# Kernel tuning notes

Measured on AMD Instinct MI355X. Metric: run time of the kernel, lower is better.

## Reference

```python
import jax, jax.numpy as jnp
import numpy as np

# dims
B, S, E, H, W = 32, 256, 512, 512, 512   # batch, max_sentence_length, word_emb, rnn_units, weight_size
ENC = 2 * H                               # bidirectional encoder hidden
V = 50000                                 # vocab


def setup_inputs() -> dict:
    key = jax.random.key(0)
    ks = jax.random.split(key, 16)
    n = jax.random.normal
    return {
        "word_ids": jax.random.randint(ks[0], (B, S), 0, V),
        "encoder_outputs": n(ks[1], (B, S, ENC), jnp.float32),
        "encoder_hn": n(ks[2], (B, H), jnp.float32),          # initial decoder cell state
        "emb": n(ks[3], (V, E), jnp.float32) * 0.02,          # WordFeature embedding table
        "chunk_emb": n(ks[4], (S, W), jnp.float32) * 0.02,    # chunk_length_embedding
        "W1": n(ks[5], (ENC, W), jnp.float32) / np.sqrt(ENC),
        "W2": n(ks[6], (E, W), jnp.float32) / np.sqrt(E),
        "W3": n(ks[7], (E, W), jnp.float32) / np.sqrt(E),
        "W4": n(ks[8], (H, W), jnp.float32) / np.sqrt(H),
        "vt1": n(ks[9], (W,), jnp.float32) / np.sqrt(W),
        "vt2": n(ks[10], (W,), jnp.float32) / np.sqrt(W),
        "Wx": n(ks[11], (E, 4 * H), jnp.float32) / np.sqrt(E),  # decoder LSTM cell
        "Wh": n(ks[12], (H, 4 * H), jnp.float32) / np.sqrt(H),
        "bias": jnp.zeros((4 * H,), jnp.float32),
    }


def reference(word_ids, encoder_outputs, encoder_hn, emb, chunk_emb,
              W1, W2, W3, W4, vt1, vt2, Wx, Wh, bias):
    Ss = word_ids.shape[1]
    Hh = encoder_hn.shape[1]
    inp = emb[word_ids]                                   # [B,S,E] word features
    b1 = jnp.einsum('bse,ew->bsw', encoder_outputs, W1)   # W1(encoder_output), hoisted
    b2 = jnp.einsum('bse,ew->bsw', inp, W2)               # W2(single_input), hoisted
    pos = jnp.arange(Ss)

    def decode_one(inp_b, b1_b, b2_b, c0):
        def step(carry, _):
            last_bond, bond, h, c, out_vec = carry
            done = bond >= Ss
            # decoder input: mean of current segment inp[last_bond:bond] (zeros at step 0)
            m = ((pos >= last_bond) & (pos < bond)).astype(inp_b.dtype)  # [S]
            x = (m @ inp_b) / jnp.maximum(m.sum(), 1.0)                  # [E]
            # LSTM cell (stand-in for decoder.pointer_forward)
            gates = x @ Wx + h @ Wh + bias                               # [4H]
            i_g, f_g, g_g, o_g = jnp.split(gates, 4)
            c_n = jax.nn.sigmoid(f_g) * c + jax.nn.sigmoid(i_g) * jnp.tanh(g_g)
            h_n = jax.nn.sigmoid(o_g) * jnp.tanh(c_n)
            h2 = jnp.where(done, h, h_n)
            c2 = jnp.where(done, c, c_n)
            bidx = jnp.minimum(bond, Ss - 1)
            # pointer attention over positions >= bond
            blend = jnp.tanh(b1_b + b2_b + inp_b[bidx] @ W3 + h2 @ W4)   # [S,W]
            seg_len = jnp.clip(bond - last_bond, 0, Ss - 1)
            scores = blend @ vt1 + chunk_emb[seg_len] @ vt2              # [S]
            scores = jnp.where(pos >= bidx, scores, -1e30)
            # log_softmax is monotonic -> argmax of scores == argmax of log-probs
            idx = jnp.argmax(scores)                                     # absolute = max_index + bond
            new_bond = jnp.where(idx > bond, idx, bond + 1)              # force progress
            widx = jnp.minimum(new_bond, Ss - 1)
            val = jnp.where((~done) & (new_bond < Ss), 1.0, out_vec[widx])
            out_new = out_vec.at[widx].set(val)
            last2 = jnp.where(done, last_bond, bond)
            bond2 = jnp.where(done, bond, new_bond)
            return (last2, bond2, h2, c2, out_new), None

        init = (jnp.int32(0), jnp.int32(0),
                jnp.zeros((Hh,), inp_b.dtype), c0,
                jnp.zeros((Ss,), inp_b.dtype))
        (_, _, _, _, out_vec), _ = jax.lax.scan(step, init, None, length=Ss)
        return out_vec

    outs = jax.vmap(decode_one)(inp, b1, b2, encoder_hn)   # [B,S]
    return outs.T                                          # [S,B] == torch.stack(output_list, 1)
```

## Files before the change

kernel.cpp:

```cpp
#include <hip/hip_runtime.h>
#include <math.h>

#define Bn   32
#define Sn   256
#define En   512
#define Hn   512
#define Wn   512
#define ENCn 1024
#define G4   2048
#define KTOT 1536

#define OFF_BSUM  0L
#define OFF_U3    4194304L
#define OFF_PE    8388608L
#define OFF_WB    12599296L
#define OFF_W4B   14696448L
#define OFF_GATES 14958592L
#define OFF_H     15089664L
#define OFF_C     15106048L
#define OFF_SPART 15138816L
#define OFF_STATE 15204352L


__device__ __forceinline__ float aload(const float* p) {
    return __hip_atomic_load(p, __ATOMIC_RELAXED, __HIP_MEMORY_SCOPE_AGENT);
}
__device__ __forceinline__ void astore(float* p, float v) {
    __hip_atomic_store(p, v, __ATOMIC_RELAXED, __HIP_MEMORY_SCOPE_AGENT);
}
__device__ __forceinline__ int aiload(const int* p) {
    return __hip_atomic_load(p, __ATOMIC_RELAXED, __HIP_MEMORY_SCOPE_AGENT);
}
__device__ __forceinline__ unsigned long long aload64(const unsigned long long* p) {
    return __hip_atomic_load(p, __ATOMIC_RELAXED, __HIP_MEMORY_SCOPE_AGENT);
}
__device__ __forceinline__ void astore64(unsigned long long* p, unsigned long long v) {
    __hip_atomic_store(p, v, __ATOMIC_RELAXED, __HIP_MEMORY_SCOPE_AGENT);
}

__global__ void init_kernel(const float* __restrict__ hn0, float* __restrict__ h,
                            float* __restrict__ c, int* __restrict__ state)
{
    int i = blockIdx.x * blockDim.x + threadIdx.x;
    if (i < Bn * Hn) { h[i] = 0.0f; c[i] = hn0[i]; }
    if (i < 8192) state[i] = (i == 1024) ? Bn : 0;
}

__global__ void wtrans_kernel(const float* __restrict__ Wx, const float* __restrict__ Wh,
                              const float* __restrict__ W4, float* __restrict__ WB,
                              float* __restrict__ W4B)
{
    int idx = blockIdx.x * 256 + threadIdx.x;
    if (idx < 2097152) {
        const int cc = idx & 3, l = (idx >> 2) & 63, kq = (idx >> 8) & 255, cb = idx >> 16;
        const int k = 4 * kq + cc, j = cb * 64 + l;
        WB[idx] = (k < 512) ? Wx[(long)k * G4 + j] : Wh[(long)(k - 512) * G4 + j];
    }
    if (idx < 262144) {
        const int cc = idx & 3, l = (idx >> 2) & 63, kq = (idx >> 8) & 127, cb = idx >> 15;
        const int k = 4 * kq + cc, j = cb * 64 + l;
        W4B[idx] = W4[(long)k * Wn + j];
    }
}

__global__ void pe1_kernel(const int* __restrict__ wid, const float* __restrict__ emb,
                           float* __restrict__ pb)
{
    const int b = blockIdx.x, blk = blockIdx.y;
    __shared__ int wids[16];
    if (threadIdx.x < 16) wids[threadIdx.x] = wid[b * Sn + blk * 16 + threadIdx.x];
    __syncthreads();
    float a0 = 0.f, a1 = 0.f;
    for (int s = 0; s < 16; ++s) {
        const float* r = emb + (long)wids[s] * En;
        a0 += r[threadIdx.x]; a1 += r[threadIdx.x + 256];
    }
    pb[((long)b * 16 + blk) * En + threadIdx.x] = a0;
    pb[((long)b * 16 + blk) * En + threadIdx.x + 256] = a1;
}

__global__ void pe2_kernel(const int* __restrict__ wid, const float* __restrict__ emb,
                           const float* __restrict__ pb, float* __restrict__ pe)
{
    const int b = blockIdx.x, blk = blockIdx.y;
    __shared__ int wids[16];
    if (threadIdx.x < 16) wids[threadIdx.x] = wid[b * Sn + blk * 16 + threadIdx.x];
    __syncthreads();
    float a0 = 0.f, a1 = 0.f;
    for (int j = 0; j < blk; ++j) {
        a0 += pb[((long)b * 16 + j) * En + threadIdx.x];
        a1 += pb[((long)b * 16 + j) * En + threadIdx.x + 256];
    }
    float* base = pe + (long)b * 257 * En;
    if (blk == 0) { base[threadIdx.x] = 0.f; base[threadIdx.x + 256] = 0.f; }
    for (int s = 0; s < 16; ++s) {
        const float* r = emb + (long)wids[s] * En;
        a0 += r[threadIdx.x]; a1 += r[threadIdx.x + 256];
        float* o = base + (long)(blk * 16 + s + 1) * En;
        o[threadIdx.x] = a0; o[threadIdx.x + 256] = a1;
    }
}

__global__ __launch_bounds__(256) void bsum_gemm(
    const float* __restrict__ enc, const int* __restrict__ wid,
    const float* __restrict__ emb, const float* __restrict__ W1,
    const float* __restrict__ W2, float* __restrict__ bsum)
{
    __shared__ float As[16][68];
    __shared__ float Bs[16][68];
    const int tid  = threadIdx.x;
    const int row0 = blockIdx.y * 64;
    const int col0 = blockIdx.x * 64;
    const int tm0  = (tid & 15) * 4;
    const int tn0  = (tid >> 4) * 4;
    const int la_r = tid >> 2;
    const int la_k = (tid & 3) * 4;
    const int lb_k = tid >> 4;
    const int lb_n = (tid & 15) * 4;

    float acc[4][4];
#pragma unroll
    for (int i = 0; i < 4; i++)
#pragma unroll
        for (int j = 0; j < 4; j++) acc[i][j] = 0.0f;

    for (int k0 = 0; k0 < KTOT; k0 += 16) {
        const int gr = row0 + la_r;
        float4 av;
        if (k0 < ENCn) {
            av = *(const float4*)&enc[(long)gr * ENCn + k0 + la_k];
        } else {
            const int wv = wid[gr];
            av = *(const float4*)&emb[(long)wv * En + (k0 - ENCn) + la_k];
        }
        As[la_k + 0][la_r] = av.x;
        As[la_k + 1][la_r] = av.y;
        As[la_k + 2][la_r] = av.z;
        As[la_k + 3][la_r] = av.w;
        float4 bv;
        if (k0 < ENCn) bv = *(const float4*)&W1[(long)(k0 + lb_k) * Wn + col0 + lb_n];
        else           bv = *(const float4*)&W2[(long)(k0 - ENCn + lb_k) * Wn + col0 + lb_n];
        *(float4*)&Bs[lb_k][lb_n] = bv;
        __syncthreads();
#pragma unroll
        for (int kk = 0; kk < 16; kk++) {
            float4 a = *(const float4*)&As[kk][tm0];
            float4 b = *(const float4*)&Bs[kk][tn0];
            acc[0][0] += a.x * b.x; acc[0][1] += a.x * b.y; acc[0][2] += a.x * b.z; acc[0][3] += a.x * b.w;
            acc[1][0] += a.y * b.x; acc[1][1] += a.y * b.y; acc[1][2] += a.y * b.z; acc[1][3] += a.y * b.w;
            acc[2][0] += a.z * b.x; acc[2][1] += a.z * b.y; acc[2][2] += a.z * b.z; acc[2][3] += a.z * b.w;
            acc[3][0] += a.w * b.x; acc[3][1] += a.w * b.y; acc[3][2] += a.w * b.z; acc[3][3] += a.w * b.w;
        }
        __syncthreads();
    }
#pragma unroll
    for (int i = 0; i < 4; i++) {
        float4 o = make_float4(acc[i][0], acc[i][1], acc[i][2], acc[i][3]);
        *(float4*)&bsum[(long)(row0 + tm0 + i) * Wn + col0 + tn0] = o;
    }
}

__global__ __launch_bounds__(256) void u3_gemm(
    const int* __restrict__ wid, const float* __restrict__ emb,
    const float* __restrict__ W3, float* __restrict__ u3)
{
    __shared__ float As[16][68];
    __shared__ float Bs[16][68];
    const int tid  = threadIdx.x;
    const int row0 = blockIdx.y * 64;
    const int col0 = blockIdx.x * 64;
    const int tm0  = (tid & 15) * 4;
    const int tn0  = (tid >> 4) * 4;
    const int la_r = tid >> 2;
    const int la_k = (tid & 3) * 4;
    const int lb_k = tid >> 4;
    const int lb_n = (tid & 15) * 4;

    float acc[4][4];
#pragma unroll
    for (int i = 0; i < 4; i++)
#pragma unroll
        for (int j = 0; j < 4; j++) acc[i][j] = 0.0f;

    for (int k0 = 0; k0 < 512; k0 += 16) {
        const int gr = row0 + la_r;
        const int wv = wid[gr];
        float4 av = *(const float4*)&emb[(long)wv * En + k0 + la_k];
        As[la_k + 0][la_r] = av.x;
        As[la_k + 1][la_r] = av.y;
        As[la_k + 2][la_r] = av.z;
        As[la_k + 3][la_r] = av.w;
        *(float4*)&Bs[lb_k][lb_n] = *(const float4*)&W3[(long)(k0 + lb_k) * Wn + col0 + lb_n];
        __syncthreads();
#pragma unroll
        for (int kk = 0; kk < 16; kk++) {
            float4 a = *(const float4*)&As[kk][tm0];
            float4 b = *(const float4*)&Bs[kk][tn0];
            acc[0][0] += a.x * b.x; acc[0][1] += a.x * b.y; acc[0][2] += a.x * b.z; acc[0][3] += a.x * b.w;
            acc[1][0] += a.y * b.x; acc[1][1] += a.y * b.y; acc[1][2] += a.y * b.z; acc[1][3] += a.y * b.w;
            acc[2][0] += a.z * b.x; acc[2][1] += a.z * b.y; acc[2][2] += a.z * b.z; acc[2][3] += a.z * b.w;
            acc[3][0] += a.w * b.x; acc[3][1] += a.w * b.y; acc[3][2] += a.w * b.z; acc[3][3] += a.w * b.w;
        }
        __syncthreads();
    }
#pragma unroll
    for (int i = 0; i < 4; i++) {
        float4 o = make_float4(acc[i][0], acc[i][1], acc[i][2], acc[i][3]);
        *(float4*)&u3[(long)(row0 + tm0 + i) * Wn + col0 + tn0] = o;
    }
}

__global__ __launch_bounds__(256) void decode_kernel(
    const float* __restrict__ bias, const float* __restrict__ vt1,
    const float* __restrict__ bsum, const float* __restrict__ u3,
    const float* __restrict__ pe,   const float* __restrict__ WB,
    const float* __restrict__ W4B,  float* __restrict__ gpart,
    float* __restrict__ hbuf, float* __restrict__ cbuf,
    float* __restrict__ spart,
    int* __restrict__ state, float* __restrict__ out)
{
    __shared__ __align__(16) float wlds[32768];
    __shared__ __align__(16) float sx[4096];
    __shared__ __align__(16) float sred[2048];
    __shared__ float s_svt[64];
    __shared__ float s_wv[4];
    __shared__ int   s_wi[4];
    __shared__ int   s_last;
    __shared__ int   s_bd[8], s_ls[8];
    __shared__ int   s_exit;

    const int wg   = blockIdx.x;
    const int tid  = threadIdx.x;
    const int lane = tid & 63;
    const int wv   = tid >> 6;

    int* gcnt = state;
    int* scnt = state + 512;
    int* nact = state + 1024;
    unsigned long long* s64b = (unsigned long long*)(state + 1536);

    const int cb1 = wg & 31;
    const int kh  = (wg >> 5) & 1;
    const int bg  = wg >> 6;
    const int b2  = wg >> 3;
    const int cb2 = wg & 7;
    const int bq2 = (wg >> 3) & 7;
    const float4* W4B4 = (const float4*)W4B;
    float4* wlds4 = (float4*)wlds;
    float4* sx4   = (float4*)sx;

    {
        const float4* src = (const float4*)WB + ((long)cb1 * 256 + kh * 128) * 64;
        for (int i = tid; i < 8192; i += 256) wlds4[i] = src[i];
    }
    if (tid < 64) s_svt[tid] = vt1[cb2 * 64 + tid];

    int a_b = 0;

    for (int t = 1; t <= Sn; ++t) {
        if (tid < 64) {
            const bool isb = tid < 8;
            const unsigned long long* sp = s64b + 8 * (bg * 8 + (tid & 7));
            for (;;) {
                unsigned long long pk = isb ? aload64(sp) : 0ULL;
                const int ep = (int)(pk & 0xffffu);
                const int bd = (int)((pk >> 16) & 0xffffu);
                const bool ok = !isb || (ep >= t - 1) || (bd >= Sn);
                int ex = 0;
                if (tid == 8) ex = (aiload(nact) == 0);
                const unsigned long long bal  = __ballot(ok);
                const unsigned long long balx = __ballot(ex != 0);
                if (((bal & 0xffULL) == 0xffULL) || balx) {
                    if (isb) { s_bd[tid] = bd; s_ls[tid] = (int)((pk >> 32) & 0xffffu); }
                    if (tid == 0) s_exit = (balx != 0ULL);
                    break;
                }
                __builtin_amdgcn_s_sleep(1);
            }
        }
        __syncthreads();
        if (s_exit) break;

        int anyact = 0;
#pragma unroll
        for (int q = 0; q < 8; ++q) anyact |= (s_bd[q] < Sn);

        if (anyact) {
            for (int idx = tid; idx < 4096; idx += 256) {
                const int bq = idx >> 9, k = idx & 511;
                const int b  = bg * 8 + bq;
                float v = 0.f;
                if (s_bd[bq] < Sn) {
                    if (kh == 0) {
                        const int bd = s_bd[bq], ls = s_ls[bq];
                        const float inv = 1.0f / (float)max(bd - ls, 1);
                        v = (pe[((long)b * 257 + bd) * En + k] - pe[((long)b * 257 + ls) * En + k]) * inv;
                    } else {
                        v = aload(&hbuf[b * Hn + k]);
                    }
                }
                sx[idx] = v;
            }
            __syncthreads();
            {
                float acc[8] = {0.f,0.f,0.f,0.f,0.f,0.f,0.f,0.f};
                const float4* wl = wlds4 + (wv * 32) * 64 + lane;
#pragma unroll 8
                for (int kq = 0; kq < 32; ++kq) {
                    const float4 w = wl[kq * 64];
                    const int kb = wv * 32 + kq;
#pragma unroll
                    for (int bq = 0; bq < 8; ++bq) {
                        const float4 xv = sx4[bq * 128 + kb];
                        acc[bq] += w.x * xv.x + w.y * xv.y + w.z * xv.z + w.w * xv.w;
                    }
                }
#pragma unroll
                for (int bq = 0; bq < 8; ++bq)
                    sred[wv * 512 + bq * 64 + lane] = acc[bq];
            }
            __syncthreads();
#pragma unroll
            for (int o = tid; o < 512; o += 256) {
                const int bq = o >> 6;
                if (s_bd[bq] < Sn) {
                    const float s = sred[o] + sred[512 + o] + sred[1024 + o] + sred[1536 + o];
                    astore(&gpart[((long)(kh * Bn) + bg * 8 + bq) * G4 + cb1 * 64 + (o & 63)], s);
                }
            }
            __syncthreads();
        }
        if (tid < 8)
            __hip_atomic_fetch_add(&gcnt[16 * (bg * 8 + tid)], 1,
                                   __ATOMIC_RELAXED, __HIP_MEMORY_SCOPE_AGENT);

        const int bd = s_bd[bq2];
        if (bd < Sn) {
            ++a_b;
            const float* cold = cbuf + ((a_b - 1) & 1) * (Bn * Hn);
            float*       cnew = cbuf + (a_b & 1) * (Bn * Hn);
            if (tid == 0) {
                while (aiload(&gcnt[16 * b2]) < 64 * t) __builtin_amdgcn_s_sleep(1);
            }
            __syncthreads();
            const float* gp0 = gpart + (long)b2 * G4;
            const float* gp1 = gpart + (long)(Bn + b2) * G4;
            for (int j = tid; j < Hn; j += 256) {
                const float ig = aload(&gp0[j])        + aload(&gp1[j])        + bias[j];
                const float fg = aload(&gp0[512 + j])  + aload(&gp1[512 + j])  + bias[512 + j];
                const float gg = aload(&gp0[1024 + j]) + aload(&gp1[1024 + j]) + bias[1024 + j];
                const float og = aload(&gp0[1536 + j]) + aload(&gp1[1536 + j]) + bias[1536 + j];
                const float co = aload(&cold[b2 * Hn + j]);
                const float sf  = 1.f / (1.f + expf(-fg));
                const float sig = 1.f / (1.f + expf(-ig));
                const float so  = 1.f / (1.f + expf(-og));
                const float cn  = sf * co + sig * tanhf(gg);
                const float h2  = so * tanhf(cn);
                sx[j] = h2;
                if (cb2 == 0) { astore(&hbuf[b2 * Hn + j], h2); astore(&cnew[b2 * Hn + j], cn); }
            }
            __syncthreads();
            {
                float acc = 0.f;
                const float4* wrow = W4B4 + ((long)cb2 * 128 + wv * 32) * 64 + lane;
#pragma unroll 8
                for (int kq = 0; kq < 32; ++kq) {
                    const float4 w  = wrow[(long)kq * 64];
                    const float4 xv = sx4[wv * 32 + kq];
                    acc += w.x * xv.x + w.y * xv.y + w.z * xv.z + w.w * xv.w;
                }
                sx[512 + wv * 64 + lane] = acc;
            }
            __syncthreads();
            if (tid < 64) {
                const float* u3row = u3 + ((long)b2 * Sn + bd) * Wn + cb2 * 64;
                sx[768 + tid] = sx[512 + tid] + sx[576 + tid] + sx[640 + tid]
                              + sx[704 + tid] + u3row[tid];
            }
            __syncthreads();
            if (tid >= bd) {
                const float* row = bsum + ((long)b2 * Sn + tid) * Wn + cb2 * 64;
                float a = 0.f;
#pragma unroll 8
                for (int i = 0; i < 64; ++i)
                    a += tanhf(row[i] + sx[768 + i]) * s_svt[i];
                astore(&spart[((long)b2 * 8 + cb2) * 256 + tid], a);
            }
            __syncthreads();
            if (tid == 0) {
                int o = __hip_atomic_fetch_add(&scnt[16 * b2], 1,
                                               __ATOMIC_RELAXED, __HIP_MEMORY_SCOPE_AGENT);
                s_last = (o == 8 * a_b - 1);
            }
            __syncthreads();
            if (s_last) {
                float v = -3.402823e38f; int vi = Sn;
                if (tid >= bd) {
                    const float* sp = spart + (long)b2 * 8 * 256 + tid;
                    float s = 0.f;
#pragma unroll
                    for (int k = 0; k < 8; ++k) s += aload(&sp[k * 256]);
                    v = s; vi = tid;
                }
#pragma unroll
                for (int off = 32; off; off >>= 1) {
                    const float v2 = __shfl_xor(v, off, 64);
                    const int   i2 = __shfl_xor(vi, off, 64);
                    if (v2 > v || (v2 == v && i2 < vi)) { v = v2; vi = i2; }
                }
                if (lane == 0) { s_wv[wv] = v; s_wi[wv] = vi; }
                __syncthreads();
                if (tid == 0) {
                    float bv = s_wv[0]; int bi = s_wi[0];
#pragma unroll
                    for (int k = 1; k < 4; ++k)
                        if (s_wv[k] > bv || (s_wv[k] == bv && s_wi[k] < bi)) { bv = s_wv[k]; bi = s_wi[k]; }
                    const int nb2 = (bi > bd) ? bi : bd + 1;
                    if (nb2 < Sn) out[nb2 * Bn + b2] = 1.0f;
                    else __hip_atomic_fetch_add(nact, -1, __ATOMIC_RELAXED, __HIP_MEMORY_SCOPE_AGENT);
                    const unsigned long long pk =
                        (unsigned long long)(unsigned)t |
                        ((unsigned long long)(unsigned)nb2 << 16) |
                        ((unsigned long long)(unsigned)bd  << 32);
                    astore64(&s64b[8 * b2], pk);
                }
            }
        }
    }
}

extern "C" void kernel_launch(void* const* d_in, const int* in_sizes, int n_in,
                              void* d_out, int out_size, void* d_ws, size_t ws_size,
                              hipStream_t stream)
{
    const int*   wid  = (const int*)d_in[0];
    const float* enc  = (const float*)d_in[1];
    const float* hn0  = (const float*)d_in[2];
    const float* emb  = (const float*)d_in[3];
    const float* W1   = (const float*)d_in[5];
    const float* W2   = (const float*)d_in[6];
    const float* W3   = (const float*)d_in[7];
    const float* W4   = (const float*)d_in[8];
    const float* vt1  = (const float*)d_in[9];
    const float* Wx   = (const float*)d_in[11];
    const float* Wh   = (const float*)d_in[12];
    const float* bias = (const float*)d_in[13];

    float* ws    = (float*)d_ws;
    float* bsum  = ws + OFF_BSUM;
    float* u3    = ws + OFF_U3;
    float* pb    = ws + OFF_U3;
    float* pe    = ws + OFF_PE;
    float* WB    = ws + OFF_WB;
    float* W4B   = ws + OFF_W4B;
    float* gpart = ws + OFF_GATES;
    float* h     = ws + OFF_H;
    float* c     = ws + OFF_C;
    float* spart = ws + OFF_SPART;
    int*   state = (int*)(ws + OFF_STATE);
    float* out   = (float*)d_out;

    hipMemsetAsync(d_out, 0, (size_t)Sn * Bn * sizeof(float), stream);
    hipLaunchKernelGGL(init_kernel, dim3(64), dim3(256), 0, stream, hn0, h, c, state);
    hipLaunchKernelGGL(wtrans_kernel, dim3(8192), dim3(256), 0, stream, Wx, Wh, W4, WB, W4B);
    hipLaunchKernelGGL(pe1_kernel, dim3(32, 16), dim3(256), 0, stream, wid, emb, pb);
    hipLaunchKernelGGL(pe2_kernel, dim3(32, 16), dim3(256), 0, stream, wid, emb, pb, pe);
    hipLaunchKernelGGL(u3_gemm, dim3(8, 128), dim3(256), 0, stream, wid, emb, W3, u3);
    hipLaunchKernelGGL(bsum_gemm, dim3(8, 128), dim3(256), 0, stream, enc, wid, emb, W1, W2, bsum);

    void* args[] = { (void*)&bias, (void*)&vt1, (void*)&bsum, (void*)&u3, (void*)&pe,
                     (void*)&WB, (void*)&W4B, (void*)&gpart, (void*)&h, (void*)&c,
                     (void*)&spart, (void*)&state, (void*)&out };
    hipLaunchCooperativeKernel((void*)decode_kernel, dim3(256), dim3(256), args, 0, stream);
}
```

Before: 865.7 us.

## Replace atomic counters with per-producer flag arrays and 64-bit packed gate exchange

Swaps the fetch_add gate and score counters for per-producer flag slots that consumers poll in parallel, so there are no atomic read-modify-write operations on one shared counter. Score reduction is now done by a fixed block that waits on flags from the other seven blocks, replacing the last-arriver election. The global active count is dropped in favour of checking whether all batch entries are done, and gate, h and c exchanges use 64-bit packed loads and stores. The cost is more polling traffic, and the fixed reducer block now sits on the critical path.

```diff
diff --git a/kernel.cpp b/kernel.cpp
--- a/kernel.cpp
+++ b/kernel.cpp
@@ -21,6 +21,7 @@
 #define OFF_SPART 15138816L
 #define OFF_STATE 15204352L
 
+typedef unsigned long long u64t;
 
 __device__ __forceinline__ float aload(const float* p) {
     return __hip_atomic_load(p, __ATOMIC_RELAXED, __HIP_MEMORY_SCOPE_AGENT);
@@ -31,19 +32,27 @@
 __device__ __forceinline__ int aiload(const int* p) {
     return __hip_atomic_load(p, __ATOMIC_RELAXED, __HIP_MEMORY_SCOPE_AGENT);
 }
-__device__ __forceinline__ unsigned long long aload64(const unsigned long long* p) {
+__device__ __forceinline__ void aistore(int* p, int v) {
+    __hip_atomic_store(p, v, __ATOMIC_RELAXED, __HIP_MEMORY_SCOPE_AGENT);
+}
+__device__ __forceinline__ u64t aload64(const u64t* p) {
     return __hip_atomic_load(p, __ATOMIC_RELAXED, __HIP_MEMORY_SCOPE_AGENT);
 }
-__device__ __forceinline__ void astore64(unsigned long long* p, unsigned long long v) {
+__device__ __forceinline__ void astore64(u64t* p, u64t v) {
     __hip_atomic_store(p, v, __ATOMIC_RELAXED, __HIP_MEMORY_SCOPE_AGENT);
 }
+__device__ __forceinline__ u64t pack2(float a, float b) {
+    return (u64t)__float_as_uint(a) | ((u64t)__float_as_uint(b) << 32);
+}
+__device__ __forceinline__ float lo32(u64t v) { return __uint_as_float((unsigned)(v & 0xffffffffu)); }
+__device__ __forceinline__ float hi32(u64t v) { return __uint_as_float((unsigned)(v >> 32)); }
 
 __global__ void init_kernel(const float* __restrict__ hn0, float* __restrict__ h,
                             float* __restrict__ c, int* __restrict__ state)
 {
     int i = blockIdx.x * blockDim.x + threadIdx.x;
     if (i < Bn * Hn) { h[i] = 0.0f; c[i] = hn0[i]; }
-    if (i < 8192) state[i] = (i == 1024) ? Bn : 0;
+    if (i < 8192) state[i] = 0;
 }
 
 __global__ void wtrans_kernel(const float* __restrict__ Wx, const float* __restrict__ Wh,
@@ -225,7 +234,6 @@
     __shared__ float s_svt[64];
     __shared__ float s_wv[4];
     __shared__ int   s_wi[4];
-    __shared__ int   s_last;
     __shared__ int   s_bd[8], s_ls[8];
     __shared__ int   s_exit;
 
@@ -234,10 +242,9 @@
     const int lane = tid & 63;
     const int wv   = tid >> 6;
 
-    int* gcnt = state;
-    int* scnt = state + 512;
-    int* nact = state + 1024;
-    unsigned long long* s64b = (unsigned long long*)(state + 1536);
+    u64t* s64   = (u64t*)state;
+    int*  garr  = state + 2560;
+    int*  sflag = state + 4608;
 
     const int cb1 = wg & 31;
     const int kh  = (wg >> 5) & 1;
@@ -248,6 +255,11 @@
     const float4* W4B4 = (const float4*)W4B;
     float4* wlds4 = (float4*)wlds;
     float4* sx4   = (float4*)sx;
+    u64t* gp64 = (u64t*)gpart;
+    u64t* h64  = (u64t*)hbuf;
+    u64t* c64  = (u64t*)cbuf;
+    const float2* pef2  = (const float2*)pe;
+    const float2* bias2 = (const float2*)bias;
 
     {
         const float4* src = (const float4*)WB + ((long)cb1 * 256 + kh * 128) * 64;
@@ -260,19 +272,18 @@
     for (int t = 1; t <= Sn; ++t) {
         if (tid < 64) {
             const bool isb = tid < 8;
-            const unsigned long long* sp = s64b + 8 * (bg * 8 + (tid & 7));
+            const u64t* sp = s64 + 768 + 16 * (bg * 8 + (tid & 7));
             for (;;) {
-                unsigned long long pk = isb ? aload64(sp) : 0ULL;
+                const u64t pk = isb ? aload64(sp) : 0ULL;
                 const int ep = (int)(pk & 0xffffu);
                 const int bd = (int)((pk >> 16) & 0xffffu);
                 const bool ok = !isb || (ep >= t - 1) || (bd >= Sn);
-                int ex = 0;
-                if (tid == 8) ex = (aiload(nact) == 0);
-                const unsigned long long bal  = __ballot(ok);
-                const unsigned long long balx = __ballot(ex != 0);
-                if (((bal & 0xffULL) == 0xffULL) || balx) {
+                const bool dn = isb && (bd >= Sn);
+                const u64t okb = __ballot(ok);
+                const u64t dnb = __ballot(dn);
+                if ((okb & 0xffULL) == 0xffULL) {
                     if (isb) { s_bd[tid] = bd; s_ls[tid] = (int)((pk >> 32) & 0xffffu); }
-                    if (tid == 0) s_exit = (balx != 0ULL);
+                    if (tid == 0) s_exit = ((dnb & 0xffULL) == 0xffULL);
                     break;
                 }
                 __builtin_amdgcn_s_sleep(1);
@@ -281,83 +292,112 @@
         __syncthreads();
         if (s_exit) break;
 
-        int anyact = 0;
-#pragma unroll
-        for (int q = 0; q < 8; ++q) anyact |= (s_bd[q] < Sn);
-
-        if (anyact) {
-            for (int idx = tid; idx < 4096; idx += 256) {
-                const int bq = idx >> 9, k = idx & 511;
-                const int b  = bg * 8 + bq;
-                float v = 0.f;
-                if (s_bd[bq] < Sn) {
-                    if (kh == 0) {
-                        const int bd = s_bd[bq], ls = s_ls[bq];
-                        const float inv = 1.0f / (float)max(bd - ls, 1);
-                        v = (pe[((long)b * 257 + bd) * En + k] - pe[((long)b * 257 + ls) * En + k]) * inv;
-                    } else {
-                        v = aload(&hbuf[b * Hn + k]);
-                    }
-                }
-                sx[idx] = v;
-            }
-            __syncthreads();
-            {
-                float acc[8] = {0.f,0.f,0.f,0.f,0.f,0.f,0.f,0.f};
-                const float4* wl = wlds4 + (wv * 32) * 64 + lane;
+        for (int idx = tid; idx < 2048; idx += 256) {
+            const int bq = idx >> 8, kp = idx & 255;
+            const int b  = bg * 8 + bq;
+            float v0 = 0.f, v1 = 0.f;
+            if (s_bd[bq] < Sn) {
+                if (kh == 0) {
+                    const int bd = s_bd[bq], ls = s_ls[bq];
+                    const float inv = 1.0f / (float)max(bd - ls, 1);
+                    const float2 pa = pef2[((long)b * 257 + bd) * 256 + kp];
+                    const float2 pb_ = pef2[((long)b * 257 + ls) * 256 + kp];
+                    v0 = (pa.x - pb_.x) * inv;
+                    v1 = (pa.y - pb_.y) * inv;
+                } else {
+                    const u64t hv = aload64(&h64[b * 256 + kp]);
+                    v0 = lo32(hv); v1 = hi32(hv);
+                }
+            }
+            sx[bq * 512 + 2 * kp]     = v0;
+            sx[bq * 512 + 2 * kp + 1] = v1;
+        }
+        __syncthreads();
+        {
+            float acc[8] = {0.f,0.f,0.f,0.f,0.f,0.f,0.f,0.f};
+            const float4* wl = wlds4 + (wv * 32) * 64 + lane;
 #pragma unroll 8
-                for (int kq = 0; kq < 32; ++kq) {
-                    const float4 w = wl[kq * 64];
-                    const int kb = wv * 32 + kq;
-#pragma unroll
-                    for (int bq = 0; bq < 8; ++bq) {
-                        const float4 xv = sx4[bq * 128 + kb];
-                        acc[bq] += w.x * xv.x + w.y * xv.y + w.z * xv.z + w.w * xv.w;
-                    }
-                }
-#pragma unroll
-                for (int bq = 0; bq < 8; ++bq)
-                    sred[wv * 512 + bq * 64 + lane] = acc[bq];
-            }
-            __syncthreads();
-#pragma unroll
-            for (int o = tid; o < 512; o += 256) {
-                const int bq = o >> 6;
-                if (s_bd[bq] < Sn) {
-                    const float s = sred[o] + sred[512 + o] + sred[1024 + o] + sred[1536 + o];
-                    astore(&gpart[((long)(kh * Bn) + bg * 8 + bq) * G4 + cb1 * 64 + (o & 63)], s);
-                }
-            }
-            __syncthreads();
-        }
+            for (int kq = 0; kq < 32; ++kq) {
+                const float4 w = wl[kq * 64];
+                const int kb = wv * 32 + kq;
+#pragma unroll
+                for (int bq = 0; bq < 8; ++bq) {
+                    const float4 xv = sx4[bq * 128 + kb];
+                    acc[bq] += w.x * xv.x + w.y * xv.y + w.z * xv.z + w.w * xv.w;
+                }
+            }
+#pragma unroll
+            for (int bq = 0; bq < 8; ++bq)
+                sred[wv * 512 + bq * 64 + lane] = acc[bq];
+        }
+        __syncthreads();
+        {
+            const int bq = tid >> 5, cp = tid & 31;
+            if (s_bd[bq] < Sn) {
+                const int c0 = 2 * cp, c1 = 2 * cp + 1;
+                const float lo = sred[bq * 64 + c0] + sred[512 + bq * 64 + c0]
+                               + sred[1024 + bq * 64 + c0] + sred[1536 + bq * 64 + c0];
+                const float hi = sred[bq * 64 + c1] + sred[512 + bq * 64 + c1]
+                               + sred[1024 + bq * 64 + c1] + sred[1536 + bq * 64 + c1];
+                astore64(&gp64[(long)(kh * Bn + bg * 8 + bq) * 1024 + cb1 * 32 + cp], pack2(lo, hi));
+            }
+        }
+        __syncthreads();
         if (tid < 8)
-            __hip_atomic_fetch_add(&gcnt[16 * (bg * 8 + tid)], 1,
-                                   __ATOMIC_RELAXED, __HIP_MEMORY_SCOPE_AGENT);
+            aistore(&garr[64 * (bg * 8 + tid) + cb1 * 2 + kh], t);
 
         const int bd = s_bd[bq2];
         if (bd < Sn) {
             ++a_b;
-            const float* cold = cbuf + ((a_b - 1) & 1) * (Bn * Hn);
-            float*       cnew = cbuf + (a_b & 1) * (Bn * Hn);
-            if (tid == 0) {
-                while (aiload(&gcnt[16 * b2]) < 64 * t) __builtin_amdgcn_s_sleep(1);
+            if (tid < 64) {
+                while (aiload(&garr[64 * b2 + tid]) < t) __builtin_amdgcn_s_sleep(1);
             }
             __syncthreads();
-            const float* gp0 = gpart + (long)b2 * G4;
-            const float* gp1 = gpart + (long)(Bn + b2) * G4;
-            for (int j = tid; j < Hn; j += 256) {
-                const float ig = aload(&gp0[j])        + aload(&gp1[j])        + bias[j];
-                const float fg = aload(&gp0[512 + j])  + aload(&gp1[512 + j])  + bias[512 + j];
-                const float gg = aload(&gp0[1024 + j]) + aload(&gp1[1024 + j]) + bias[1024 + j];
-                const float og = aload(&gp0[1536 + j]) + aload(&gp1[1536 + j]) + bias[1536 + j];
-                const float co = aload(&cold[b2 * Hn + j]);
-                const float sf  = 1.f / (1.f + expf(-fg));
-                const float sig = 1.f / (1.f + expf(-ig));
-                const float so  = 1.f / (1.f + expf(-og));
-                const float cn  = sf * co + sig * tanhf(gg);
-                const float h2  = so * tanhf(cn);
-                sx[j] = h2;
-                if (cb2 == 0) { astore(&hbuf[b2 * Hn + j], h2); astore(&cnew[b2 * Hn + j], cn); }
+            {
+                const long base0 = (long)b2 * 1024;
+                const long base1 = (long)(Bn + b2) * 1024;
+                const u64t gi0 = aload64(&gp64[base0 + 0 * 256 + tid]);
+                const u64t gf0 = aload64(&gp64[base0 + 1 * 256 + tid]);
+                const u64t gg0 = aload64(&gp64[base0 + 2 * 256 + tid]);
+                const u64t go0 = aload64(&gp64[base0 + 3 * 256 + tid]);
+                const u64t gi1 = aload64(&gp64[base1 + 0 * 256 + tid]);
+                const u64t gf1 = aload64(&gp64[base1 + 1 * 256 + tid]);
+                const u64t gg1 = aload64(&gp64[base1 + 2 * 256 + tid]);
+                const u64t go1 = aload64(&gp64[base1 + 3 * 256 + tid]);
+                const u64t cv  = aload64(&c64[((a_b - 1) & 1) * 8192 + b2 * 256 + tid]);
+                const float2 bi = bias2[0 * 256 + tid];
+                const float2 bf = bias2[1 * 256 + tid];
+                const float2 bg_ = bias2[2 * 256 + tid];
+                const float2 bo = bias2[3 * 256 + tid];
+                float h2a, h2b, cna, cnb;
+                {
+                    const float ig = lo32(gi0) + lo32(gi1) + bi.x;
+                    const float fg = lo32(gf0) + lo32(gf1) + bf.x;
+                    const float gg = lo32(gg0) + lo32(gg1) + bg_.x;
+                    const float og = lo32(go0) + lo32(go1) + bo.x;
+                    const float sf = 1.f / (1.f + expf(-fg));
+                    const float si = 1.f / (1.f + expf(-ig));
+                    const float so = 1.f / (1.f + expf(-og));
+                    cna = sf * lo32(cv) + si * tanhf(gg);
+                    h2a = so * tanhf(cna);
+                }
+                {
+                    const float ig = hi32(gi0) + hi32(gi1) + bi.y;
+                    const float fg = hi32(gf0) + hi32(gf1) + bf.y;
+                    const float gg = hi32(gg0) + hi32(gg1) + bg_.y;
+                    const float og = hi32(go0) + hi32(go1) + bo.y;
+                    const float sf = 1.f / (1.f + expf(-fg));
+                    const float si = 1.f / (1.f + expf(-ig));
+                    const float so = 1.f / (1.f + expf(-og));
+                    cnb = sf * hi32(cv) + si * tanhf(gg);
+                    h2b = so * tanhf(cnb);
+                }
+                sx[2 * tid]     = h2a;
+                sx[2 * tid + 1] = h2b;
+                if (cb2 == 0) {
+                    astore64(&h64[b2 * 256 + tid], pack2(h2a, h2b));
+                    astore64(&c64[(a_b & 1) * 8192 + b2 * 256 + tid], pack2(cna, cnb));
+                }
             }
             __syncthreads();
             {
@@ -387,13 +427,13 @@
                 astore(&spart[((long)b2 * 8 + cb2) * 256 + tid], a);
             }
             __syncthreads();
-            if (tid == 0) {
-                int o = __hip_atomic_fetch_add(&scnt[16 * b2], 1,
-                                               __ATOMIC_RELAXED, __HIP_MEMORY_SCOPE_AGENT);
-                s_last = (o == 8 * a_b - 1);
-            }
-            __syncthreads();
-            if (s_last) {
+            if (cb2 != 0) {
+                if (tid == 0) aistore(&sflag[16 * b2 + cb2], a_b);
+            } else {
+                if (tid >= 1 && tid < 8) {
+                    while (aiload(&sflag[16 * b2 + tid]) < a_b) __builtin_amdgcn_s_sleep(1);
+                }
+                __syncthreads();
                 float v = -3.402823e38f; int vi = Sn;
                 if (tid >= bd) {
                     const float* sp = spart + (long)b2 * 8 * 256 + tid;
@@ -411,18 +451,17 @@
                 if (lane == 0) { s_wv[wv] = v; s_wi[wv] = vi; }
                 __syncthreads();
                 if (tid == 0) {
-                    float bv = s_wv[0]; int bi = s_wi[0];
+                    float bv = s_wv[0]; int bi_ = s_wi[0];
 #pragma unroll
                     for (int k = 1; k < 4; ++k)
-                        if (s_wv[k] > bv || (s_wv[k] == bv && s_wi[k] < bi)) { bv = s_wv[k]; bi = s_wi[k]; }
-                    const int nb2 = (bi > bd) ? bi : bd + 1;
+                        if (s_wv[k] > bv || (s_wv[k] == bv && s_wi[k] < bi_)) { bv = s_wv[k]; bi_ = s_wi[k]; }
+                    const int nb2 = (bi_ > bd) ? bi_ : bd + 1;
                     if (nb2 < Sn) out[nb2 * Bn + b2] = 1.0f;
-                    else __hip_atomic_fetch_add(nact, -1, __ATOMIC_RELAXED, __HIP_MEMORY_SCOPE_AGENT);
-                    const unsigned long long pk =
-                        (unsigned long long)(unsigned)t |
-                        ((unsigned long long)(unsigned)nb2 << 16) |
-                        ((unsigned long long)(unsigned)bd  << 32);
-                    astore64(&s64b[8 * b2], pk);
+                    const u64t pk =
+                        (u64t)(unsigned)t |
+                        ((u64t)(unsigned)nb2 << 16) |
+                        ((u64t)(unsigned)bd  << 32);
+                    astore64(&s64[768 + 16 * b2], pk);
                 }
             }
         }
```

New measurement: 800.5 us. 7.5% less time.
